# Performance work log

Hardware: AMD Instinct MI355X
Metric: run time of the kernel (lower is better)

## Reference

```python
import jax, jax.numpy as jnp
import numpy as np
import math

D_MODEL = 512
D_STATE = 64  # N; state uses N//2 complex modes
BATCH = 8
SEQ = 4096
DT_MIN, DT_MAX = 1e-3, 1e-1


def setup_inputs() -> dict:
    key = jax.random.key(0)
    ks = jax.random.split(key, 8)
    H, N2 = D_MODEL, D_STATE // 2
    x = jax.random.normal(ks[0], (BATCH, SEQ, D_MODEL), dtype=jnp.float32)
    log_dt = jax.random.uniform(ks[1], (H,), dtype=jnp.float32) * (math.log(DT_MAX) - math.log(DT_MIN)) + math.log(DT_MIN)
    # A = -0.5 + i*pi*n  ->  A_real_log = log(0.5)
    A_real_log = jnp.full((H, N2), math.log(0.5), dtype=jnp.float32)
    A_imag = jnp.tile(jnp.arange(N2, dtype=jnp.float32) * math.pi, (H, 1))
    B_re = jax.random.normal(ks[2], (H, N2), dtype=jnp.float32)
    B_im = jax.random.normal(ks[3], (H, N2), dtype=jnp.float32)
    C_re = jax.random.normal(ks[4], (H, N2), dtype=jnp.float32)
    C_im = jax.random.normal(ks[5], (H, N2), dtype=jnp.float32)
    D = jax.random.normal(ks[6], (H,), dtype=jnp.float32)
    return {"x": x, "log_dt": log_dt, "A_real_log": A_real_log, "A_imag": A_imag,
            "B_re": B_re, "B_im": B_im, "C_re": C_re, "C_im": C_im, "D": D}


def _s4d_scan(x, log_dt, A_real_log, A_imag, B_re, B_im, C_re, C_im, D):
    # ZOH discretization (setup_step)
    dt = jnp.exp(log_dt)                                 # (H,)
    A = -jnp.exp(A_real_log) + 1j * A_imag               # (H, N2) complex
    dtA = A * dt[:, None]
    dA = jnp.exp(dtA)                                    # (H, N2)
    Bc = B_re + 1j * B_im
    Cc = C_re + 1j * C_im
    dB = Bc * (jnp.expm1(dtA) / A)                       # (H, N2)

    Bsz = x.shape[0]
    state0 = jnp.zeros((Bsz, x.shape[2], dA.shape[1]), dtype=jnp.complex64)

    def step(state, x_t):  # x_t: (B, H)
        state = dA * state + dB * x_t[..., None]         # (B, H, N2)
        y = 2.0 * jnp.real(jnp.einsum('hn,bhn->bh', Cc, state)) + D * x_t
        return state, jax.nn.gelu(y, approximate=False)

    final_state, ys = jax.lax.scan(step, state0, jnp.swapaxes(x, 0, 1))  # ys: (L, B, H)
    return jnp.swapaxes(ys, 0, 1), final_state


def reference(x, log_dt, A_real_log, A_imag, B_re, B_im, C_re, C_im, D):
    return _s4d_scan(x, log_dt, A_real_log, A_imag, B_re, B_im, C_re, C_im, D)
```

## Files before the change

### kernel.cpp

```cpp
#include <hip/hip_runtime.h>
#include <math.h>


#define H_  512
#define L_  4096
#define B_  8
#define N2_ 32
#define NC  64
#define THREADS 256
#define COLS 256
#define RSTR 72

typedef _Float16 f16;
typedef _Float16 f16x8 __attribute__((ext_vector_type(8)));
typedef _Float16 f16x4 __attribute__((ext_vector_type(4)));
typedef float    f32x4 __attribute__((ext_vector_type(4)));

__device__ __forceinline__ float bfly1(float v) {
    return __int_as_float(__builtin_amdgcn_update_dpp(
        0, __float_as_int(v), 0xB1, 0xf, 0xf, true));
}

__global__ __launch_bounds__(256) void k_trin(
    const float* __restrict__ x, f16* __restrict__ xT)
{
    __shared__ float tl[64][65];
    const int bid = (int)blockIdx.x;
    const int tt = bid & 63, hh = (bid >> 6) & 7, b = bid >> 9;
    const int t0 = tt * 64, h0 = hh * 64;
    const int tid = threadIdx.x;

    const float* src = x + ((size_t)b * L_ + t0) * H_ + h0;
#pragma unroll
    for (int i = 0; i < 4; ++i) {
        const int e = i * 256 + tid;
        const int t = e >> 4, hq = e & 15;
        const f32x4 v = *(const f32x4*)&src[(size_t)t * H_ + hq * 4];
#pragma unroll
        for (int j = 0; j < 4; ++j) tl[hq * 4 + j][t] = v[j];
    }
    __syncthreads();
#pragma unroll
    for (int i = 0; i < 2; ++i) {
        const int e = i * 256 + tid;
        const int hI = e >> 3, tq = e & 7;
        f16x8 pk;
#pragma unroll
        for (int j = 0; j < 8; ++j) pk[j] = (f16)tl[hI][tq * 8 + j];
        *(f16x8*)&xT[((size_t)(h0 + hI) * B_ + b) * L_ + t0 + tq * 8] = pk;
    }
}

__global__ __launch_bounds__(256) void k_trout(
    const f16* __restrict__ yT, float* __restrict__ y)
{
    __shared__ float tl[64][65];
    const int bid = (int)blockIdx.x;
    const int tt = bid & 63, hh = (bid >> 6) & 7, b = bid >> 9;
    const int t0 = tt * 64, h0 = hh * 64;
    const int tid = threadIdx.x;

#pragma unroll
    for (int i = 0; i < 2; ++i) {
        const int e = i * 256 + tid;
        const int hI = e >> 3, tq = e & 7;
        const f16x8 v = *(const f16x8*)
            &yT[((size_t)(h0 + hI) * B_ + b) * L_ + t0 + tq * 8];
#pragma unroll
        for (int j = 0; j < 8; ++j) tl[tq * 8 + j][hI] = (float)v[j];
    }
    __syncthreads();
    float* dst = y + ((size_t)b * L_ + t0) * H_ + h0;
#pragma unroll
    for (int i = 0; i < 4; ++i) {
        const int e = i * 256 + tid;
        const int t = e >> 4, hq = e & 15;
        f32x4 v;
#pragma unroll
        for (int j = 0; j < 4; ++j) v[j] = tl[t][hq * 4 + j];
        *(f32x4*)&dst[(size_t)t * H_ + hq * 4] = v;
    }
}

__global__ __launch_bounds__(256) void k_build(
    const float* __restrict__ log_dt,
    const float* __restrict__ A_real_log,
    const float* __restrict__ A_imag,
    const float* __restrict__ B_re,
    const float* __restrict__ B_im,
    const float* __restrict__ C_re,
    const float* __restrict__ C_im,
    f16*  __restrict__ G,
    float* __restrict__ Lg)
{
    __shared__ float pr[32 * 66], pi[32 * 66];
    __shared__ float s_xr[32], s_xi[32], s_dBr[32], s_dBi[32],
                     s_wr[32], s_wi[32], s_wdr[32], s_wdi[32], s_k[64];
    const int h   = (int)blockIdx.x;
    const int tid = threadIdx.x;

    if (tid < 32) {
        const int n = tid, hn = h * N2_ + n;
        const float dt = expf(log_dt[h]);
        const float Ar = -expf(A_real_log[hn]);
        const float Ai = A_imag[hn];
        const float xr = dt * Ar, xi = dt * Ai;
        s_xr[n] = xr; s_xi[n] = xi;
        const float ex = expf(xr), cs = cosf(xi), sn = sinf(xi);
        const float sh  = sinf(0.5f * xi);
        const float emr = expm1f(xr) * cs - 2.0f * sh * sh;
        const float emi = ex * sn;
        const float ia  = 1.0f / (Ar * Ar + Ai * Ai);
        const float tr  = (emr * Ar + emi * Ai) * ia;
        const float ti  = (emi * Ar - emr * Ai) * ia;
        const float Brv = B_re[hn], Biv = B_im[hn];
        const float dBr = Brv * tr - Biv * ti, dBi = Brv * ti + Biv * tr;
        s_dBr[n] = dBr; s_dBi[n] = dBi;
        const float wr = 2.0f * C_re[hn], wi = 2.0f * C_im[hn];
        s_wr[n] = wr; s_wi[n] = wi;
        s_wdr[n] = wr * dBr - wi * dBi;
        s_wdi[n] = wr * dBi + wi * dBr;
    }
    __syncthreads();

    for (int e = tid; e < 2048; e += 256) {
        const int n = e >> 6, p = e & 63;
        const float ex = expf((float)p * s_xr[n]);
        float sn, cs; sincosf((float)p * s_xi[n], &sn, &cs);
        pr[n * 66 + p] = ex * cs; pi[n * 66 + p] = ex * sn;
    }
    if (tid < 32) {
        const int n = tid;
        const float ex = expf(64.f * s_xr[n]);
        float sn, cs; sincosf(64.f * s_xi[n], &sn, &cs);
        pr[n * 66 + 64] = ex * cs; pi[n * 66 + 64] = ex * sn;
    }
    __syncthreads();

    if (tid < 64) {
        float acc = 0.f;
        for (int n = 0; n < 32; ++n)
            acc += s_wdr[n] * pr[n * 66 + tid] - s_wdi[n] * pi[n * 66 + tid];
        s_k[tid] = acc;
    }
    if (tid < 32) {
        Lg[h * 64 + tid]      = pr[tid * 66 + 64];
        Lg[h * 64 + 32 + tid] = pi[tid * 66 + 64];
    }
    f16* Gh = G + (size_t)h * 192 * 64;
    for (int e = tid; e < 4096; e += 256) {
        const int t = e >> 6, j = e & 63, n = j >> 1;
        const float re = pr[n * 66 + t + 1], im = pi[n * 66 + t + 1];
        const float mv = (j & 1) ? -(s_wr[n] * im + s_wi[n] * re)
                                 :  (s_wr[n] * re - s_wi[n] * im);
        Gh[(size_t)(64 + t) * 64 + j] = (f16)mv;
    }
    for (int e = tid; e < 4096; e += 256) {
        const int r = e >> 6, s = e & 63, n = r >> 1;
        const float re = pr[n * 66 + 63 - s], im = pi[n * 66 + 63 - s];
        const float vv = (r & 1) ? (s_dBr[n] * im + s_dBi[n] * re)
                                 : (s_dBr[n] * re - s_dBi[n] * im);
        Gh[(size_t)(128 + r) * 64 + s] = (f16)vv;
    }
    __syncthreads();
    for (int e = tid; e < 4096; e += 256) {
        const int t = e >> 6, s = e & 63;
        Gh[(size_t)t * 64 + s] = (f16)((s <= t) ? s_k[t - s] : 0.f);
    }
}

__global__ __launch_bounds__(THREADS, 2) void s4d_conv_kernel(
    const f16*  __restrict__ xT,
    const f16*  __restrict__ G,
    const float* __restrict__ Lg,
    const float* __restrict__ Dv,
    f16*  __restrict__ yT,
    float* __restrict__ st_re,
    float* __restrict__ st_im)
{
    __shared__ f16 Xl[COLS][RSTR];
    __shared__ f16 PU[COLS][RSTR];
    __shared__ float s_Lr[32], s_Li[32];

    const int bid = (int)blockIdx.x;
    const int li  = bid >> 3;
    const int h   = (bid & 7) * 64 + (li >> 1);
    const int bh  = li & 1;

    const int tid = threadIdx.x;
    const int l   = tid & 63;
    const int w   = tid >> 6;

    const float Dh = Dv[h];

    {
        const f16* Gh = G + (size_t)h * 192 * 64;
        for (int e = tid; e < 1536; e += THREADS) {
            const int row = e >> 3, seg = e & 7;
            *(f16x8*)&Xl[row][seg * 8] =
                *(const f16x8*)&Gh[(size_t)row * 64 + seg * 8];
        }
        if (tid < 32) {
            s_Lr[tid] = Lg[h * 64 + tid];
            s_Li[tid] = Lg[h * 64 + 32 + tid];
        }
    }
    __syncthreads();

    const int row16 = l & 15, kg = l >> 4;
    f16x8 Tf[4][2], Mf[4][2], Vf[4][2];
#pragma unroll
    for (int mt = 0; mt < 4; ++mt)
#pragma unroll
        for (int ks = 0; ks < 2; ++ks) {
            const int off = ks * 32 + kg * 8;
            Tf[mt][ks] = *(const f16x8*)&Xl[      mt * 16 + row16][off];
            Mf[mt][ks] = *(const f16x8*)&Xl[ 64 + mt * 16 + row16][off];
            Vf[mt][ks] = *(const f16x8*)&Xl[128 + mt * 16 + row16][off];
        }
    __syncthreads();

    {
        const int col = tid, b = bh * 4 + (col >> 6), c = col & 63;
        const f16* xg = xT + ((size_t)h * B_ + b) * L_ + (size_t)c * 64;
#pragma unroll
        for (int s0 = 0; s0 < 64; s0 += 8)
            *(f16x8*)&Xl[col][s0] = *(const f16x8*)&xg[s0];
    }
    __syncthreads();

    const int colbase = w * 64;

    f16x8 xbA[4], xbB[4];
#pragma unroll
    for (int nt = 0; nt < 4; ++nt) {
        const int col = colbase + nt * 16 + row16;
        xbA[nt] = *(const f16x8*)&Xl[col][kg * 8];
        xbB[nt] = *(const f16x8*)&Xl[col][32 + kg * 8];
        f32x4 ac0 = {0.f,0.f,0.f,0.f}, ac1 = {0.f,0.f,0.f,0.f},
              ac2 = {0.f,0.f,0.f,0.f}, ac3 = {0.f,0.f,0.f,0.f};
        ac0 = __builtin_amdgcn_mfma_f32_16x16x32_f16(Vf[0][0], xbA[nt], ac0, 0,0,0);
        ac0 = __builtin_amdgcn_mfma_f32_16x16x32_f16(Vf[0][1], xbB[nt], ac0, 0,0,0);
        ac1 = __builtin_amdgcn_mfma_f32_16x16x32_f16(Vf[1][0], xbA[nt], ac1, 0,0,0);
        ac1 = __builtin_amdgcn_mfma_f32_16x16x32_f16(Vf[1][1], xbB[nt], ac1, 0,0,0);
        ac2 = __builtin_amdgcn_mfma_f32_16x16x32_f16(Vf[2][0], xbA[nt], ac2, 0,0,0);
        ac2 = __builtin_amdgcn_mfma_f32_16x16x32_f16(Vf[2][1], xbB[nt], ac2, 0,0,0);
        ac3 = __builtin_amdgcn_mfma_f32_16x16x32_f16(Vf[3][0], xbA[nt], ac3, 0,0,0);
        ac3 = __builtin_amdgcn_mfma_f32_16x16x32_f16(Vf[3][1], xbB[nt], ac3, 0,0,0);
        f32x4 a4[4] = {ac0, ac1, ac2, ac3};
#pragma unroll
        for (int mt = 0; mt < 4; ++mt) {
            f16x4 pv;
            pv[0] = (f16)a4[mt][0]; pv[1] = (f16)a4[mt][1];
            pv[2] = (f16)a4[mt][2]; pv[3] = (f16)a4[mt][3];
            *(f16x4*)&PU[col][mt * 16 + kg * 4] = pv;
        }
    }

    {
        const int j = l, n = j >> 1;
        const float lr  = s_Lr[n];
        const float lis = (j & 1) ? s_Li[n] : -s_Li[n];
        float u = 0.f;
        for (int c0 = 0; c0 < NC; c0 += 8) {
            float pv[8];
#pragma unroll
            for (int k2 = 0; k2 < 8; ++k2)
                pv[k2] = (float)PU[colbase + c0 + k2][j];
#pragma unroll
            for (int k2 = 0; k2 < 8; ++k2) {
                PU[colbase + c0 + k2][j] = (f16)u;
                const float usw = bfly1(u);
                u = fmaf(lr, u, fmaf(lis, usw, pv[k2]));
            }
        }
        const int pairIdx = (bh * 4 + w) * H_ + h;
        if ((j & 1) == 0) st_re[(size_t)pairIdx * N2_ + n] = u;
        else              st_im[(size_t)pairIdx * N2_ + n] = u;
    }

    {
        const int b = bh * 4 + w;
        f16* yb = yT + ((size_t)h * B_ + b) * L_;
#pragma unroll
        for (int nt = 0; nt < 4; ++nt) {
            const int col = colbase + nt * 16 + row16;
            const int cc  = nt * 16 + row16;
            const f16x8 ub0 = *(const f16x8*)&PU[col][kg * 8];
            const f16x8 ub1 = *(const f16x8*)&PU[col][32 + kg * 8];
#pragma unroll
            for (int mt = 0; mt < 4; ++mt) {
                f32x4 ac = {0.f, 0.f, 0.f, 0.f};
                ac = __builtin_amdgcn_mfma_f32_16x16x32_f16(Tf[mt][0], xbA[nt], ac, 0,0,0);
                ac = __builtin_amdgcn_mfma_f32_16x16x32_f16(Tf[mt][1], xbB[nt], ac, 0,0,0);
                ac = __builtin_amdgcn_mfma_f32_16x16x32_f16(Mf[mt][0], ub0, ac, 0,0,0);
                ac = __builtin_amdgcn_mfma_f32_16x16x32_f16(Mf[mt][1], ub1, ac, 0,0,0);
                const int t0 = mt * 16 + kg * 4;
                const f16x4 xs = *(const f16x4*)&Xl[col][t0];
                f16x4 pk;
#pragma unroll
                for (int r = 0; r < 4; ++r) {
                    const float y  = fmaf(Dh, (float)xs[r], ac[r]);
                    const float y2 = y * y;
                    const float arg = y * fmaf(-0.10294502f, y2, -2.30218425f);
                    const float e   = __builtin_amdgcn_exp2f(arg);
                    pk[r] = (f16)(y * __builtin_amdgcn_rcpf(1.0f + e));
                }
                *(f16x4*)&yb[(size_t)cc * 64 + t0] = pk;
            }
        }
    }
}

extern "C" void kernel_launch(void* const* d_in, const int* in_sizes, int n_in,
                              void* d_out, int out_size, void* d_ws, size_t ws_size,
                              hipStream_t stream) {
    (void)in_sizes; (void)n_in; (void)out_size; (void)ws_size;
    const float* x    = (const float*)d_in[0];
    const float* ldt  = (const float*)d_in[1];
    const float* Arl  = (const float*)d_in[2];
    const float* Aim  = (const float*)d_in[3];
    const float* Bre  = (const float*)d_in[4];
    const float* Bim  = (const float*)d_in[5];
    const float* Cre  = (const float*)d_in[6];
    const float* Cim  = (const float*)d_in[7];
    const float* Dv   = (const float*)d_in[8];
    float* out = (float*)d_out;
    float* st_re = out + (size_t)B_ * L_ * H_;
    float* st_im = st_re + (size_t)B_ * H_ * N2_;

    f16*   xT = (f16*)out;
    f16*   G  = (f16*)((char*)out + 33554432);
    float* Lg = (float*)((char*)out + 33554432 + (size_t)H_ * 192 * 64 * 2);
    f16*   yT = (f16*)d_ws;

    hipLaunchKernelGGL(k_trin, dim3(64 * 8 * B_), dim3(256), 0, stream, x, xT);
    hipLaunchKernelGGL(k_build, dim3(H_), dim3(256), 0, stream,
                       ldt, Arl, Aim, Bre, Bim, Cre, Cim, G, Lg);
    hipLaunchKernelGGL(s4d_conv_kernel, dim3(1024), dim3(THREADS), 0, stream,
                       xT, G, Lg, Dv, yT, st_re, st_im);
    hipLaunchKernelGGL(k_trout, dim3(64 * 8 * B_), dim3(256), 0, stream,
                       yT, out);
}
```

Before: 174.6 us.

## Fuse transpose and build kernels, fold D into Toeplitz, share one LDS buffer

```diff
diff --git a/kernel.cpp b/kernel.cpp
--- a/kernel.cpp
+++ b/kernel.cpp
@@ -21,68 +21,9 @@
         0, __float_as_int(v), 0xB1, 0xf, 0xf, true));
 }
 
-__global__ __launch_bounds__(256) void k_trin(
-    const float* __restrict__ x, f16* __restrict__ xT)
-{
-    __shared__ float tl[64][65];
-    const int bid = (int)blockIdx.x;
-    const int tt = bid & 63, hh = (bid >> 6) & 7, b = bid >> 9;
-    const int t0 = tt * 64, h0 = hh * 64;
-    const int tid = threadIdx.x;
-
-    const float* src = x + ((size_t)b * L_ + t0) * H_ + h0;
-#pragma unroll
-    for (int i = 0; i < 4; ++i) {
-        const int e = i * 256 + tid;
-        const int t = e >> 4, hq = e & 15;
-        const f32x4 v = *(const f32x4*)&src[(size_t)t * H_ + hq * 4];
-#pragma unroll
-        for (int j = 0; j < 4; ++j) tl[hq * 4 + j][t] = v[j];
-    }
-    __syncthreads();
-#pragma unroll
-    for (int i = 0; i < 2; ++i) {
-        const int e = i * 256 + tid;
-        const int hI = e >> 3, tq = e & 7;
-        f16x8 pk;
-#pragma unroll
-        for (int j = 0; j < 8; ++j) pk[j] = (f16)tl[hI][tq * 8 + j];
-        *(f16x8*)&xT[((size_t)(h0 + hI) * B_ + b) * L_ + t0 + tq * 8] = pk;
-    }
-}
-
-__global__ __launch_bounds__(256) void k_trout(
-    const f16* __restrict__ yT, float* __restrict__ y)
-{
-    __shared__ float tl[64][65];
-    const int bid = (int)blockIdx.x;
-    const int tt = bid & 63, hh = (bid >> 6) & 7, b = bid >> 9;
-    const int t0 = tt * 64, h0 = hh * 64;
-    const int tid = threadIdx.x;
-
-#pragma unroll
-    for (int i = 0; i < 2; ++i) {
-        const int e = i * 256 + tid;
-        const int hI = e >> 3, tq = e & 7;
-        const f16x8 v = *(const f16x8*)
-            &yT[((size_t)(h0 + hI) * B_ + b) * L_ + t0 + tq * 8];
-#pragma unroll
-        for (int j = 0; j < 8; ++j) tl[tq * 8 + j][hI] = (float)v[j];
-    }
-    __syncthreads();
-    float* dst = y + ((size_t)b * L_ + t0) * H_ + h0;
-#pragma unroll
-    for (int i = 0; i < 4; ++i) {
-        const int e = i * 256 + tid;
-        const int t = e >> 4, hq = e & 15;
-        f32x4 v;
-#pragma unroll
-        for (int j = 0; j < 4; ++j) v[j] = tl[t][hq * 4 + j];
-        *(f32x4*)&dst[(size_t)t * H_ + hq * 4] = v;
-    }
-}
-
-__global__ __launch_bounds__(256) void k_build(
+__global__ __launch_bounds__(256) void k_pre(
+    const float* __restrict__ x,
+    f16*  __restrict__ xT,
     const float* __restrict__ log_dt,
     const float* __restrict__ A_real_log,
     const float* __restrict__ A_imag,
@@ -90,14 +31,50 @@
     const float* __restrict__ B_im,
     const float* __restrict__ C_re,
     const float* __restrict__ C_im,
+    const float* __restrict__ Dv,
     f16*  __restrict__ G,
     float* __restrict__ Lg)
 {
-    __shared__ float pr[32 * 66], pi[32 * 66];
-    __shared__ float s_xr[32], s_xi[32], s_dBr[32], s_dBi[32],
-                     s_wr[32], s_wi[32], s_wdr[32], s_wdi[32], s_k[64];
-    const int h   = (int)blockIdx.x;
+    __shared__ __align__(16) float smem[4608];
+    const int bid = (int)blockIdx.x;
     const int tid = threadIdx.x;
+
+    if (bid < 4096) {
+        float (*tl)[65] = (float (*)[65])smem;
+        const int tt = bid & 63, hh = (bid >> 6) & 7, b = bid >> 9;
+        const int t0 = tt * 64, h0 = hh * 64;
+
+        const float* src = x + ((size_t)b * L_ + t0) * H_ + h0;
+#pragma unroll
+        for (int i = 0; i < 4; ++i) {
+            const int e = i * 256 + tid;
+            const int t = e >> 4, hq = e & 15;
+            const f32x4 v = *(const f32x4*)&src[(size_t)t * H_ + hq * 4];
+#pragma unroll
+            for (int j = 0; j < 4; ++j) tl[hq * 4 + j][t] = v[j];
+        }
+        __syncthreads();
+#pragma unroll
+        for (int i = 0; i < 2; ++i) {
+            const int e = i * 256 + tid;
+            const int hI = e >> 3, tq = e & 7;
+            f16x8 pk;
+#pragma unroll
+            for (int j = 0; j < 8; ++j) pk[j] = (f16)tl[hI][tq * 8 + j];
+            *(f16x8*)&xT[((size_t)(h0 + hI) * B_ + b) * L_ + t0 + tq * 8] = pk;
+        }
+        return;
+    }
+
+    const int h = bid - 4096;
+    float* pr = smem;
+    float* pi = smem + 2112;
+    float* sx = smem + 4224;
+    float* s_xr = sx;        float* s_xi = sx + 32;
+    float* s_dBr = sx + 64;  float* s_dBi = sx + 96;
+    float* s_wr = sx + 128;  float* s_wi = sx + 160;
+    float* s_wdr = sx + 192; float* s_wdi = sx + 224;
+    float* s_k = sx + 256;
 
     if (tid < 32) {
         const int n = tid, hn = h * N2_ + n;
@@ -147,6 +124,7 @@
         Lg[h * 64 + tid]      = pr[tid * 66 + 64];
         Lg[h * 64 + 32 + tid] = pi[tid * 66 + 64];
     }
+    const float Dh = Dv[h];
     f16* Gh = G + (size_t)h * 192 * 64;
     for (int e = tid; e < 4096; e += 256) {
         const int t = e >> 6, j = e & 63, n = j >> 1;
@@ -165,21 +143,51 @@
     __syncthreads();
     for (int e = tid; e < 4096; e += 256) {
         const int t = e >> 6, s = e & 63;
-        Gh[(size_t)t * 64 + s] = (f16)((s <= t) ? s_k[t - s] : 0.f);
-    }
-}
-
-__global__ __launch_bounds__(THREADS, 2) void s4d_conv_kernel(
+        const float tv = (s <= t) ? (s_k[t - s] + (s == t ? Dh : 0.f)) : 0.f;
+        Gh[(size_t)t * 64 + s] = (f16)tv;
+    }
+}
+
+__global__ __launch_bounds__(256) void k_trout(
+    const f16* __restrict__ yT, float* __restrict__ y)
+{
+    __shared__ float tl[64][65];
+    const int bid = (int)blockIdx.x;
+    const int tt = bid & 63, hh = (bid >> 6) & 7, b = bid >> 9;
+    const int t0 = tt * 64, h0 = hh * 64;
+    const int tid = threadIdx.x;
+
+#pragma unroll
+    for (int i = 0; i < 2; ++i) {
+        const int e = i * 256 + tid;
+        const int hI = e >> 3, tq = e & 7;
+        const f16x8 v = *(const f16x8*)
+            &yT[((size_t)(h0 + hI) * B_ + b) * L_ + t0 + tq * 8];
+#pragma unroll
+        for (int j = 0; j < 8; ++j) tl[tq * 8 + j][hI] = (float)v[j];
+    }
+    __syncthreads();
+    float* dst = y + ((size_t)b * L_ + t0) * H_ + h0;
+#pragma unroll
+    for (int i = 0; i < 4; ++i) {
+        const int e = i * 256 + tid;
+        const int t = e >> 4, hq = e & 15;
+        f32x4 v;
+#pragma unroll
+        for (int j = 0; j < 4; ++j) v[j] = tl[t][hq * 4 + j];
+        *(f32x4*)&dst[(size_t)t * H_ + hq * 4] = v;
+    }
+}
+
+__global__ __launch_bounds__(THREADS, 4) void s4d_conv_kernel(
     const f16*  __restrict__ xT,
     const f16*  __restrict__ G,
     const float* __restrict__ Lg,
-    const float* __restrict__ Dv,
     f16*  __restrict__ yT,
     float* __restrict__ st_re,
     float* __restrict__ st_im)
 {
-    __shared__ f16 Xl[COLS][RSTR];
-    __shared__ f16 PU[COLS][RSTR];
+    __shared__ f16 XP[COLS][RSTR];
     __shared__ float s_Lr[32], s_Li[32];
 
     const int bid = (int)blockIdx.x;
@@ -191,13 +199,11 @@
     const int l   = tid & 63;
     const int w   = tid >> 6;
 
-    const float Dh = Dv[h];
-
     {
         const f16* Gh = G + (size_t)h * 192 * 64;
         for (int e = tid; e < 1536; e += THREADS) {
             const int row = e >> 3, seg = e & 7;
-            *(f16x8*)&Xl[row][seg * 8] =
+            *(f16x8*)&XP[row][seg * 8] =
                 *(const f16x8*)&Gh[(size_t)row * 64 + seg * 8];
         }
         if (tid < 32) {
@@ -214,9 +220,9 @@
 #pragma unroll
         for (int ks = 0; ks < 2; ++ks) {
             const int off = ks * 32 + kg * 8;
-            Tf[mt][ks] = *(const f16x8*)&Xl[      mt * 16 + row16][off];
-            Mf[mt][ks] = *(const f16x8*)&Xl[ 64 + mt * 16 + row16][off];
-            Vf[mt][ks] = *(const f16x8*)&Xl[128 + mt * 16 + row16][off];
+            Tf[mt][ks] = *(const f16x8*)&XP[      mt * 16 + row16][off];
+            Mf[mt][ks] = *(const f16x8*)&XP[ 64 + mt * 16 + row16][off];
+            Vf[mt][ks] = *(const f16x8*)&XP[128 + mt * 16 + row16][off];
         }
     __syncthreads();
 
@@ -225,9 +231,8 @@
         const f16* xg = xT + ((size_t)h * B_ + b) * L_ + (size_t)c * 64;
 #pragma unroll
         for (int s0 = 0; s0 < 64; s0 += 8)
-            *(f16x8*)&Xl[col][s0] = *(const f16x8*)&xg[s0];
-    }
-    __syncthreads();
+            *(f16x8*)&XP[col][s0] = *(const f16x8*)&xg[s0];
+    }
 
     const int colbase = w * 64;
 
@@ -235,8 +240,8 @@
 #pragma unroll
     for (int nt = 0; nt < 4; ++nt) {
         const int col = colbase + nt * 16 + row16;
-        xbA[nt] = *(const f16x8*)&Xl[col][kg * 8];
-        xbB[nt] = *(const f16x8*)&Xl[col][32 + kg * 8];
+        xbA[nt] = *(const f16x8*)&XP[col][kg * 8];
+        xbB[nt] = *(const f16x8*)&XP[col][32 + kg * 8];
         f32x4 ac0 = {0.f,0.f,0.f,0.f}, ac1 = {0.f,0.f,0.f,0.f},
               ac2 = {0.f,0.f,0.f,0.f}, ac3 = {0.f,0.f,0.f,0.f};
         ac0 = __builtin_amdgcn_mfma_f32_16x16x32_f16(Vf[0][0], xbA[nt], ac0, 0,0,0);
@@ -253,7 +258,7 @@
             f16x4 pv;
             pv[0] = (f16)a4[mt][0]; pv[1] = (f16)a4[mt][1];
             pv[2] = (f16)a4[mt][2]; pv[3] = (f16)a4[mt][3];
-            *(f16x4*)&PU[col][mt * 16 + kg * 4] = pv;
+            *(f16x4*)&XP[col][mt * 16 + kg * 4] = pv;
         }
     }
 
@@ -266,10 +271,10 @@
             float pv[8];
 #pragma unroll
             for (int k2 = 0; k2 < 8; ++k2)
-                pv[k2] = (float)PU[colbase + c0 + k2][j];
+                pv[k2] = (float)XP[colbase + c0 + k2][j];
 #pragma unroll
             for (int k2 = 0; k2 < 8; ++k2) {
-                PU[colbase + c0 + k2][j] = (f16)u;
+                XP[colbase + c0 + k2][j] = (f16)u;
                 const float usw = bfly1(u);
                 u = fmaf(lr, u, fmaf(lis, usw, pv[k2]));
             }
@@ -286,8 +291,8 @@
         for (int nt = 0; nt < 4; ++nt) {
             const int col = colbase + nt * 16 + row16;
             const int cc  = nt * 16 + row16;
-            const f16x8 ub0 = *(const f16x8*)&PU[col][kg * 8];
-            const f16x8 ub1 = *(const f16x8*)&PU[col][32 + kg * 8];
+            const f16x8 ub0 = *(const f16x8*)&XP[col][kg * 8];
+            const f16x8 ub1 = *(const f16x8*)&XP[col][32 + kg * 8];
 #pragma unroll
             for (int mt = 0; mt < 4; ++mt) {
                 f32x4 ac = {0.f, 0.f, 0.f, 0.f};
@@ -296,11 +301,10 @@
                 ac = __builtin_amdgcn_mfma_f32_16x16x32_f16(Mf[mt][0], ub0, ac, 0,0,0);
                 ac = __builtin_amdgcn_mfma_f32_16x16x32_f16(Mf[mt][1], ub1, ac, 0,0,0);
                 const int t0 = mt * 16 + kg * 4;
-                const f16x4 xs = *(const f16x4*)&Xl[col][t0];
                 f16x4 pk;
 #pragma unroll
                 for (int r = 0; r < 4; ++r) {
-                    const float y  = fmaf(Dh, (float)xs[r], ac[r]);
+                    const float y  = ac[r];
                     const float y2 = y * y;
                     const float arg = y * fmaf(-0.10294502f, y2, -2.30218425f);
                     const float e   = __builtin_amdgcn_exp2f(arg);
@@ -334,11 +338,10 @@
     float* Lg = (float*)((char*)out + 33554432 + (size_t)H_ * 192 * 64 * 2);
     f16*   yT = (f16*)d_ws;
 
-    hipLaunchKernelGGL(k_trin, dim3(64 * 8 * B_), dim3(256), 0, stream, x, xT);
-    hipLaunchKernelGGL(k_build, dim3(H_), dim3(256), 0, stream,
-                       ldt, Arl, Aim, Bre, Bim, Cre, Cim, G, Lg);
+    hipLaunchKernelGGL(k_pre, dim3(4096 + H_), dim3(256), 0, stream,
+                       x, xT, ldt, Arl, Aim, Bre, Bim, Cre, Cim, Dv, G, Lg);
     hipLaunchKernelGGL(s4d_conv_kernel, dim3(1024), dim3(THREADS), 0, stream,
-                       xT, G, Lg, Dv, yT, st_re, st_im);
+                       xT, G, Lg, yT, st_re, st_im);
     hipLaunchKernelGGL(k_trout, dim3(64 * 8 * B_), dim3(256), 0, stream,
                        yT, out);
 }
```

Result: no change. 172.8 us (-1.0%).

## Fuse input/output transposes into chunked-scan conv kernel and fold D into Toeplitz

Applied to the files above, without the earlier changes.

```diff
diff --git a/kernel.cpp b/kernel.cpp
--- a/kernel.cpp
+++ b/kernel.cpp
@@ -7,79 +7,17 @@
 #define B_  8
 #define N2_ 32
 #define NC  64
-#define THREADS 256
-#define COLS 256
 #define RSTR 72
 
 typedef _Float16 f16;
 typedef _Float16 f16x8 __attribute__((ext_vector_type(8)));
 typedef _Float16 f16x4 __attribute__((ext_vector_type(4)));
+typedef _Float16 f16x2 __attribute__((ext_vector_type(2)));
 typedef float    f32x4 __attribute__((ext_vector_type(4)));
 
 __device__ __forceinline__ float bfly1(float v) {
     return __int_as_float(__builtin_amdgcn_update_dpp(
         0, __float_as_int(v), 0xB1, 0xf, 0xf, true));
-}
-
-__global__ __launch_bounds__(256) void k_trin(
-    const float* __restrict__ x, f16* __restrict__ xT)
-{
-    __shared__ float tl[64][65];
-    const int bid = (int)blockIdx.x;
-    const int tt = bid & 63, hh = (bid >> 6) & 7, b = bid >> 9;
-    const int t0 = tt * 64, h0 = hh * 64;
-    const int tid = threadIdx.x;
-
-    const float* src = x + ((size_t)b * L_ + t0) * H_ + h0;
-#pragma unroll
-    for (int i = 0; i < 4; ++i) {
-        const int e = i * 256 + tid;
-        const int t = e >> 4, hq = e & 15;
-        const f32x4 v = *(const f32x4*)&src[(size_t)t * H_ + hq * 4];
-#pragma unroll
-        for (int j = 0; j < 4; ++j) tl[hq * 4 + j][t] = v[j];
-    }
-    __syncthreads();
-#pragma unroll
-    for (int i = 0; i < 2; ++i) {
-        const int e = i * 256 + tid;
-        const int hI = e >> 3, tq = e & 7;
-        f16x8 pk;
-#pragma unroll
-        for (int j = 0; j < 8; ++j) pk[j] = (f16)tl[hI][tq * 8 + j];
-        *(f16x8*)&xT[((size_t)(h0 + hI) * B_ + b) * L_ + t0 + tq * 8] = pk;
-    }
-}
-
-__global__ __launch_bounds__(256) void k_trout(
-    const f16* __restrict__ yT, float* __restrict__ y)
-{
-    __shared__ float tl[64][65];
-    const int bid = (int)blockIdx.x;
-    const int tt = bid & 63, hh = (bid >> 6) & 7, b = bid >> 9;
-    const int t0 = tt * 64, h0 = hh * 64;
-    const int tid = threadIdx.x;
-
-#pragma unroll
-    for (int i = 0; i < 2; ++i) {
-        const int e = i * 256 + tid;
-        const int hI = e >> 3, tq = e & 7;
-        const f16x8 v = *(const f16x8*)
-            &yT[((size_t)(h0 + hI) * B_ + b) * L_ + t0 + tq * 8];
-#pragma unroll
-        for (int j = 0; j < 8; ++j) tl[tq * 8 + j][hI] = (float)v[j];
-    }
-    __syncthreads();
-    float* dst = y + ((size_t)b * L_ + t0) * H_ + h0;
-#pragma unroll
-    for (int i = 0; i < 4; ++i) {
-        const int e = i * 256 + tid;
-        const int t = e >> 4, hq = e & 15;
-        f32x4 v;
-#pragma unroll
-        for (int j = 0; j < 4; ++j) v[j] = tl[t][hq * 4 + j];
-        *(f32x4*)&dst[(size_t)t * H_ + hq * 4] = v;
-    }
 }
 
 __global__ __launch_bounds__(256) void k_build(
@@ -90,6 +28,7 @@
     const float* __restrict__ B_im,
     const float* __restrict__ C_re,
     const float* __restrict__ C_im,
+    const float* __restrict__ Dv,
     f16*  __restrict__ G,
     float* __restrict__ Lg)
 {
@@ -147,6 +86,7 @@
         Lg[h * 64 + tid]      = pr[tid * 66 + 64];
         Lg[h * 64 + 32 + tid] = pi[tid * 66 + 64];
     }
+    const float Dh = Dv[h];
     f16* Gh = G + (size_t)h * 192 * 64;
     for (int e = tid; e < 4096; e += 256) {
         const int t = e >> 6, j = e & 63, n = j >> 1;
@@ -165,78 +105,70 @@
     __syncthreads();
     for (int e = tid; e < 4096; e += 256) {
         const int t = e >> 6, s = e & 63;
-        Gh[(size_t)t * 64 + s] = (f16)((s <= t) ? s_k[t - s] : 0.f);
-    }
-}
-
-__global__ __launch_bounds__(THREADS, 2) void s4d_conv_kernel(
-    const f16*  __restrict__ xT,
+        const float tv = (s <= t) ? (s_k[t - s] + (s == t ? Dh : 0.f)) : 0.f;
+        Gh[(size_t)t * 64 + s] = (f16)tv;
+    }
+}
+
+__global__ __launch_bounds__(512, 4) void s4d_conv_kernel(
+    const float* __restrict__ x,
     const f16*  __restrict__ G,
     const float* __restrict__ Lg,
-    const float* __restrict__ Dv,
-    f16*  __restrict__ yT,
+    float* __restrict__ y,
     float* __restrict__ st_re,
     float* __restrict__ st_im)
 {
-    __shared__ f16 Xl[COLS][RSTR];
-    __shared__ f16 PU[COLS][RSTR];
-    __shared__ float s_Lr[32], s_Li[32];
+    __shared__ f16 XT[8][64][RSTR];
 
     const int bid = (int)blockIdx.x;
-    const int li  = bid >> 3;
-    const int h   = (bid & 7) * 64 + (li >> 1);
-    const int bh  = li & 1;
+    const int lb  = (bid & 7) * 64 + (bid >> 3);
+    const int hg  = lb >> 3;
+    const int b   = lb & 7;
 
     const int tid = threadIdx.x;
     const int l   = tid & 63;
     const int w   = tid >> 6;
-
-    const float Dh = Dv[h];
-
-    {
-        const f16* Gh = G + (size_t)h * 192 * 64;
-        for (int e = tid; e < 1536; e += THREADS) {
-            const int row = e >> 3, seg = e & 7;
-            *(f16x8*)&Xl[row][seg * 8] =
-                *(const f16x8*)&Gh[(size_t)row * 64 + seg * 8];
-        }
-        if (tid < 32) {
-            s_Lr[tid] = Lg[h * 64 + tid];
-            s_Li[tid] = Lg[h * 64 + 32 + tid];
-        }
-    }
-    __syncthreads();
-
+    const int h   = hg * 8 + w;
     const int row16 = l & 15, kg = l >> 4;
-    f16x8 Tf[4][2], Mf[4][2], Vf[4][2];
+
+    const f16* Gh = G + (size_t)h * 192 * 64;
+
+    f16x8 Vf[4][2];
 #pragma unroll
     for (int mt = 0; mt < 4; ++mt)
 #pragma unroll
-        for (int ks = 0; ks < 2; ++ks) {
-            const int off = ks * 32 + kg * 8;
-            Tf[mt][ks] = *(const f16x8*)&Xl[      mt * 16 + row16][off];
-            Mf[mt][ks] = *(const f16x8*)&Xl[ 64 + mt * 16 + row16][off];
-            Vf[mt][ks] = *(const f16x8*)&Xl[128 + mt * 16 + row16][off];
-        }
-    __syncthreads();
-
-    {
-        const int col = tid, b = bh * 4 + (col >> 6), c = col & 63;
-        const f16* xg = xT + ((size_t)h * B_ + b) * L_ + (size_t)c * 64;
-#pragma unroll
-        for (int s0 = 0; s0 < 64; s0 += 8)
-            *(f16x8*)&Xl[col][s0] = *(const f16x8*)&xg[s0];
-    }
-    __syncthreads();
-
-    const int colbase = w * 64;
+        for (int ks = 0; ks < 2; ++ks)
+            Vf[mt][ks] = *(const f16x8*)
+                &Gh[(size_t)(128 + mt * 16 + row16) * 64 + ks * 32 + kg * 8];
+    const float lr  = Lg[h * 64 + (l >> 1)];
+    const float li0 = Lg[h * 64 + 32 + (l >> 1)];
+    const float lis = (l & 1) ? li0 : -li0;
+
+    const int h_off = (tid & 1) * 4;
+    const int tp    = tid >> 1;
+    const float* xb_ = x + (size_t)b * L_ * H_ + hg * 8;
+#pragma unroll 2
+    for (int iter = 0; iter < 8; ++iter) {
+        const int t0 = iter * 512 + tp * 2;
+        const f32x4 v0 = *(const f32x4*)&xb_[(size_t)t0 * H_ + h_off];
+        const f32x4 v1 = *(const f32x4*)&xb_[(size_t)(t0 + 1) * H_ + h_off];
+        const int c = t0 >> 6, s0 = t0 & 63;
+#pragma unroll
+        for (int j = 0; j < 4; ++j) {
+            f16x2 p; p[0] = (f16)v0[j]; p[1] = (f16)v1[j];
+            *(f16x2*)&XT[h_off + j][c][s0] = p;
+        }
+    }
+    __syncthreads();
+
+    f16 (*Xw)[RSTR] = XT[w];
 
     f16x8 xbA[4], xbB[4];
 #pragma unroll
     for (int nt = 0; nt < 4; ++nt) {
-        const int col = colbase + nt * 16 + row16;
-        xbA[nt] = *(const f16x8*)&Xl[col][kg * 8];
-        xbB[nt] = *(const f16x8*)&Xl[col][32 + kg * 8];
+        const int col = nt * 16 + row16;
+        xbA[nt] = *(const f16x8*)&Xw[col][kg * 8];
+        xbB[nt] = *(const f16x8*)&Xw[col][32 + kg * 8];
         f32x4 ac0 = {0.f,0.f,0.f,0.f}, ac1 = {0.f,0.f,0.f,0.f},
               ac2 = {0.f,0.f,0.f,0.f}, ac3 = {0.f,0.f,0.f,0.f};
         ac0 = __builtin_amdgcn_mfma_f32_16x16x32_f16(Vf[0][0], xbA[nt], ac0, 0,0,0);
@@ -247,67 +179,90 @@
         ac2 = __builtin_amdgcn_mfma_f32_16x16x32_f16(Vf[2][1], xbB[nt], ac2, 0,0,0);
         ac3 = __builtin_amdgcn_mfma_f32_16x16x32_f16(Vf[3][0], xbA[nt], ac3, 0,0,0);
         ac3 = __builtin_amdgcn_mfma_f32_16x16x32_f16(Vf[3][1], xbB[nt], ac3, 0,0,0);
-        f32x4 a4[4] = {ac0, ac1, ac2, ac3};
+        const f32x4 a4[4] = {ac0, ac1, ac2, ac3};
 #pragma unroll
         for (int mt = 0; mt < 4; ++mt) {
             f16x4 pv;
             pv[0] = (f16)a4[mt][0]; pv[1] = (f16)a4[mt][1];
             pv[2] = (f16)a4[mt][2]; pv[3] = (f16)a4[mt][3];
-            *(f16x4*)&PU[col][mt * 16 + kg * 4] = pv;
+            *(f16x4*)&Xw[col][mt * 16 + kg * 4] = pv;
         }
     }
 
     {
         const int j = l, n = j >> 1;
-        const float lr  = s_Lr[n];
-        const float lis = (j & 1) ? s_Li[n] : -s_Li[n];
         float u = 0.f;
         for (int c0 = 0; c0 < NC; c0 += 8) {
             float pv[8];
 #pragma unroll
             for (int k2 = 0; k2 < 8; ++k2)
-                pv[k2] = (float)PU[colbase + c0 + k2][j];
+                pv[k2] = (float)Xw[c0 + k2][j];
 #pragma unroll
             for (int k2 = 0; k2 < 8; ++k2) {
-                PU[colbase + c0 + k2][j] = (f16)u;
+                Xw[c0 + k2][j] = (f16)u;
                 const float usw = bfly1(u);
                 u = fmaf(lr, u, fmaf(lis, usw, pv[k2]));
             }
         }
-        const int pairIdx = (bh * 4 + w) * H_ + h;
+        const int pairIdx = b * H_ + h;
         if ((j & 1) == 0) st_re[(size_t)pairIdx * N2_ + n] = u;
         else              st_im[(size_t)pairIdx * N2_ + n] = u;
     }
 
     {
-        const int b = bh * 4 + w;
-        f16* yb = yT + ((size_t)h * B_ + b) * L_;
+        f16x8 ub0[4], ub1[4];
 #pragma unroll
         for (int nt = 0; nt < 4; ++nt) {
-            const int col = colbase + nt * 16 + row16;
-            const int cc  = nt * 16 + row16;
-            const f16x8 ub0 = *(const f16x8*)&PU[col][kg * 8];
-            const f16x8 ub1 = *(const f16x8*)&PU[col][32 + kg * 8];
-#pragma unroll
-            for (int mt = 0; mt < 4; ++mt) {
+            const int col = nt * 16 + row16;
+            ub0[nt] = *(const f16x8*)&Xw[col][kg * 8];
+            ub1[nt] = *(const f16x8*)&Xw[col][32 + kg * 8];
+        }
+#pragma unroll
+        for (int mt = 0; mt < 4; ++mt) {
+            const size_t rT = (size_t)(mt * 16 + row16) * 64;
+            const size_t rM = (size_t)(64 + mt * 16 + row16) * 64;
+            const f16x8 Tf0 = *(const f16x8*)&Gh[rT + kg * 8];
+            const f16x8 Tf1 = *(const f16x8*)&Gh[rT + 32 + kg * 8];
+            const f16x8 Mf0 = *(const f16x8*)&Gh[rM + kg * 8];
+            const f16x8 Mf1 = *(const f16x8*)&Gh[rM + 32 + kg * 8];
+#pragma unroll
+            for (int nt = 0; nt < 4; ++nt) {
+                const int col = nt * 16 + row16;
                 f32x4 ac = {0.f, 0.f, 0.f, 0.f};
-                ac = __builtin_amdgcn_mfma_f32_16x16x32_f16(Tf[mt][0], xbA[nt], ac, 0,0,0);
-                ac = __builtin_amdgcn_mfma_f32_16x16x32_f16(Tf[mt][1], xbB[nt], ac, 0,0,0);
-                ac = __builtin_amdgcn_mfma_f32_16x16x32_f16(Mf[mt][0], ub0, ac, 0,0,0);
-                ac = __builtin_amdgcn_mfma_f32_16x16x32_f16(Mf[mt][1], ub1, ac, 0,0,0);
+                ac = __builtin_amdgcn_mfma_f32_16x16x32_f16(Tf0, xbA[nt], ac, 0,0,0);
+                ac = __builtin_amdgcn_mfma_f32_16x16x32_f16(Tf1, xbB[nt], ac, 0,0,0);
+                ac = __builtin_amdgcn_mfma_f32_16x16x32_f16(Mf0, ub0[nt], ac, 0,0,0);
+                ac = __builtin_amdgcn_mfma_f32_16x16x32_f16(Mf1, ub1[nt], ac, 0,0,0);
                 const int t0 = mt * 16 + kg * 4;
-                const f16x4 xs = *(const f16x4*)&Xl[col][t0];
                 f16x4 pk;
 #pragma unroll
                 for (int r = 0; r < 4; ++r) {
-                    const float y  = fmaf(Dh, (float)xs[r], ac[r]);
-                    const float y2 = y * y;
-                    const float arg = y * fmaf(-0.10294502f, y2, -2.30218425f);
+                    const float yv = ac[r];
+                    const float y2 = yv * yv;
+                    const float arg = yv * fmaf(-0.10294502f, y2, -2.30218425f);
                     const float e   = __builtin_amdgcn_exp2f(arg);
-                    pk[r] = (f16)(y * __builtin_amdgcn_rcpf(1.0f + e));
+                    pk[r] = (f16)(yv * __builtin_amdgcn_rcpf(1.0f + e));
                 }
-                *(f16x4*)&yb[(size_t)cc * 64 + t0] = pk;
+                *(f16x4*)&Xw[col][t0] = pk;
             }
+        }
+    }
+    __syncthreads();
+
+    {
+        float* yb_ = y + (size_t)b * L_ * H_ + hg * 8;
+#pragma unroll 2
+        for (int iter = 0; iter < 8; ++iter) {
+            const int t0 = iter * 512 + tp * 2;
+            const int c = t0 >> 6, s0 = t0 & 63;
+            f32x4 v0, v1;
+#pragma unroll
+            for (int j = 0; j < 4; ++j) {
+                const f16x2 p = *(const f16x2*)&XT[h_off + j][c][s0];
+                v0[j] = (float)p[0]; v1[j] = (float)p[1];
+            }
+            *(f32x4*)&yb_[(size_t)t0 * H_ + h_off]       = v0;
+            *(f32x4*)&yb_[(size_t)(t0 + 1) * H_ + h_off] = v1;
         }
     }
 }
@@ -329,16 +284,11 @@
     float* st_re = out + (size_t)B_ * L_ * H_;
     float* st_im = st_re + (size_t)B_ * H_ * N2_;
 
-    f16*   xT = (f16*)out;
-    f16*   G  = (f16*)((char*)out + 33554432);
-    float* Lg = (float*)((char*)out + 33554432 + (size_t)H_ * 192 * 64 * 2);
-    f16*   yT = (f16*)d_ws;
-
-    hipLaunchKernelGGL(k_trin, dim3(64 * 8 * B_), dim3(256), 0, stream, x, xT);
+    f16*   G  = (f16*)d_ws;
+    float* Lg = (float*)((char*)d_ws + (size_t)H_ * 192 * 64 * 2);
+
     hipLaunchKernelGGL(k_build, dim3(H_), dim3(256), 0, stream,
-                       ldt, Arl, Aim, Bre, Bim, Cre, Cim, G, Lg);
-    hipLaunchKernelGGL(s4d_conv_kernel, dim3(1024), dim3(THREADS), 0, stream,
-                       xT, G, Lg, Dv, yT, st_re, st_im);
-    hipLaunchKernelGGL(k_trout, dim3(64 * 8 * B_), dim3(256), 0, stream,
-                       yT, out);
-}
+                       ldt, Arl, Aim, Bre, Bim, Cre, Cim, Dv, G, Lg);
+    hipLaunchKernelGGL(s4d_conv_kernel, dim3(512), dim3(512), 0, stream,
+                       x, G, Lg, out, st_re, st_im);
+}
```

Measured after the change: 162.3 us. 1.08x faster.
